# Optimization experiments

Hardware: AMD Instinct MI355X
Metric: run time of the kernel (lower is better)

## Reference

```python
import jax, jax.numpy as jnp
import numpy as np
from jax import lax

B, C, H, W = 8, 2, 1024, 1024
K = 500            # max_num
POST_MAX = 83      # circle_nms post_max_size
NMS_THRESH = 4.0   # squared-distance threshold in grid units
SCORE_THR = 0.1
# post_center_range converted to grid units per CenterPointBBoxCoder.__init__
PCR_LOW = jnp.array([-100.0, -100.0, -10.0], dtype=jnp.float32)
PCR_HIGH = jnp.array([1124.0, 1124.0, 10.0], dtype=jnp.float32)


def setup_inputs() -> dict:
    key = jax.random.key(0)
    ks = jax.random.split(key, 7)
    return {
        "heat": jax.random.uniform(ks[0], (B, C, H, W), dtype=jnp.float32),
        "reg": jax.random.normal(ks[1], (B, 2, H, W), dtype=jnp.float32),
        "rot_sine": jax.random.normal(ks[2], (B, 1, H, W), dtype=jnp.float32),
        "rot_cosine": jax.random.normal(ks[3], (B, 1, H, W), dtype=jnp.float32),
        "hei": jax.random.normal(ks[4], (B, 1, H, W), dtype=jnp.float32),
        "dim": jax.random.normal(ks[5], (B, 3, H, W), dtype=jnp.float32),
        "vel": jax.random.normal(ks[6], (B, 2, H, W), dtype=jnp.float32),
    }


def _gather_feat(feat_bnc, inds_bk):
    # feat: [B, N, Ch], inds: [B, K] -> [B, K, Ch]
    return jnp.take_along_axis(feat_bnc, inds_bk[:, :, None], axis=1)


def _transpose_and_gather(feat_bchw, inds_bk):
    # [B, Ch, H, W] -> gather at flat HW indices -> [B, K, Ch]
    b, c, h, w = feat_bchw.shape
    f = feat_bchw.transpose(0, 2, 3, 1).reshape(b, h * w, c)
    return _gather_feat(f, inds_bk)


def _topk(scores):
    # scores: [B, C, H, W]
    b, c, h, w = scores.shape
    topk_scores, topk_inds = lax.top_k(scores.reshape(b, c, h * w), K)  # [B,C,K]
    topk_inds = topk_inds % (h * w)
    topk_ys = (topk_inds // w).astype(jnp.float32)
    topk_xs = (topk_inds % w).astype(jnp.float32)
    topk_score, topk_ind = lax.top_k(topk_scores.reshape(b, c * K), K)  # [B,K]
    topk_clses = (topk_ind // K).astype(jnp.int32)
    gather2 = lambda t: jnp.take_along_axis(t.reshape(b, c * K), topk_ind, axis=1)
    return topk_score, gather2(topk_inds), topk_clses, gather2(topk_ys), gather2(topk_xs)


def _circle_nms_keep(x, y, s):
    # Sequential circle NMS per image (jit-compatible fori_loop).
    k = x.shape[0]
    order = jnp.argsort(-s)
    xs, ys = x[order], y[order]
    idx = jnp.arange(k)

    def body(i, supp):
        d2 = (xs - xs[i]) ** 2 + (ys - ys[i]) ** 2
        new = supp | ((idx > i) & (d2 <= NMS_THRESH))
        return jnp.where(supp[i], supp, new)

    supp = lax.fori_loop(0, k, body, jnp.zeros(k, dtype=bool))
    keep_sorted = ~supp
    keep_sorted = keep_sorted & (jnp.cumsum(keep_sorted.astype(jnp.int32)) <= POST_MAX)
    return jnp.zeros(k, dtype=bool).at[order].set(keep_sorted)


def reference(heat, reg, rot_sine, rot_cosine, hei, dim, vel):
    scores, inds, clses, ys, xs = _topk(heat)            # [B,K] each
    reg_g = _transpose_and_gather(reg, inds)             # [B,K,2]
    xs = xs[:, :, None] + reg_g[:, :, 0:1]
    ys = ys[:, :, None] + reg_g[:, :, 1:2]
    rot = jnp.arctan2(_transpose_and_gather(rot_sine, inds),
                      _transpose_and_gather(rot_cosine, inds))  # [B,K,1]
    hei_g = _transpose_and_gather(hei, inds)             # [B,K,1]
    dim_g = _transpose_and_gather(dim, inds)             # [B,K,3]
    vel_g = _transpose_and_gather(vel, inds)             # [B,K,2]
    boxes = jnp.concatenate([xs, ys, hei_g, dim_g, rot, vel_g], axis=2)  # [B,K,9]

    valid = (boxes[..., :3] >= PCR_LOW).all(-1) & (boxes[..., :3] <= PCR_HIGH).all(-1)
    valid = valid & (scores > SCORE_THR)

    nms_scores = jnp.where(valid, scores, -1e9)
    keep = jax.vmap(_circle_nms_keep)(boxes[..., 0], boxes[..., 1], nms_scores) & valid
    return boxes, scores, clses.astype(jnp.float32), valid, keep
```

## Files before the change

### kernel.cpp

```cpp
#include <hip/hip_runtime.h>
#include <stdint.h>

typedef unsigned int u32;
typedef unsigned long long u64;

#define HW (1024*1024)
#define KTOP 500
#define CAP 8192u
#define POST_MAX 83
#define DELTA_THR 9728u

#define WS_CNT2  0
#define WS_CAND  32768
#define WS_SORT  1081344


__global__ __launch_bounds__(256) void k1_collect(const float* __restrict__ heat,
                                                  u32* cnt2, uint2* cand){
  __shared__ uint2 lbuf[64];
  __shared__ u32 lcnt;
  int s     = blockIdx.x >> 7;
  int chunk = blockIdx.x & 127;
  int tid   = threadIdx.x;
  if (tid == 0) lcnt = 0;
  __syncthreads();
  const float4* hp = (const float4*)(heat + (size_t)s*HW + (size_t)chunk*8192);
  float4 v[8];
  #pragma unroll
  for (int i = 0; i < 8; ++i) v[i] = hp[i*256 + tid];
  #pragma unroll
  for (int i = 0; i < 8; ++i){
    u32 idx0 = (u32)chunk*8192u + (u32)(i*256 + tid)*4u;
    float vals[4] = {v[i].x, v[i].y, v[i].z, v[i].w};
    #pragma unroll
    for (int c = 0; c < 4; ++c){
      u32 bits  = __float_as_uint(vals[c]);
      u32 delta = 0x3F800000u - bits;
      if (delta < DELTA_THR){
        u32 p = atomicAdd(&lcnt, 1u);
        if (p < 64u) lbuf[p] = make_uint2(bits, idx0 + (u32)c);
      }
    }
  }
  __syncthreads();
  u32 n = lcnt;
  u32 stored = (n < 64u) ? n : 64u;
  if (tid < stored) cand[(size_t)s*CAP + (u32)chunk*64u + tid] = lbuf[tid];
  if (tid == 0) cnt2[s*128 + chunk] = stored | ((n > 64u) ? 0x80000000u : 0u);
}

__global__ __launch_bounds__(1024) void kR_rank(const float* __restrict__ heat,
                                                const u32* __restrict__ cnt2,
                                                uint2* cand, uint2* sorted){
  __shared__ __align__(16) u64 lkey[CAP];
  __shared__ u32 coff[129];
  __shared__ u32 lhist[256];
  __shared__ u32 lc;
  __shared__ int t2s;
  __shared__ u32 meta;
  int s = blockIdx.x >> 1, h = blockIdx.x & 1, t = threadIdx.x;

  if (t == 0){
    u32 tot = 0, ov = 0;
    for (int c = 0; c < 128; ++c){
      u32 w = cnt2[s*128 + c];
      ov |= (w >> 31);
      coff[c] = tot;
      tot += (w & 0x7FFFFFFFu);
    }
    coff[128] = tot;
    meta = tot | (ov << 31);
  }
  __syncthreads();
  u32 total = meta & 0x7FFFFFFFu;
  bool fb = ((meta >> 31) != 0u) || (total < (u32)KTOP);
  u32 n;

  if (!fb){
    n = total;
    for (u32 i = t; i < CAP; i += 1024){
      u32 c = i >> 6, j = i & 63u;
      u32 cnt_c = coff[c+1] - coff[c];
      if (j < cnt_c){
        uint2 cv = cand[(size_t)s*CAP + i];
        lkey[coff[c] + j] = ((u64)(~cv.x) << 32) | (u64)cv.y;
      }
    }
    __syncthreads();
  } else {
    if (h) return;
    if (t < 256) lhist[t] = 0;
    if (t == 0) lc = 0;
    __syncthreads();
    const float4* hp = (const float4*)(heat + (size_t)s*HW);
    for (int it = 0; it < 256; ++it){
      float4 v = hp[it*1024 + t];
      #pragma unroll
      for (int c = 0; c < 4; ++c){
        float val = (c==0)?v.x:(c==1)?v.y:(c==2)?v.z:v.w;
        u32 bits  = __float_as_uint(val);
        u32 delta = 0x3F800000u - bits;
        u32 bin   = delta >> 16; if (bin > 255u) bin = 255u;
        atomicAdd(&lhist[bin], 1u);
      }
    }
    __syncthreads();
    if (t == 0){
      u32 cum = 0; u32 b1 = 255u;
      for (u32 bb = 0; bb < 256u; ++bb){
        cum += lhist[bb];
        if (cum >= (u32)KTOP){ b1 = bb; break; }
      }
      t2s = (int)(0x3F800000u - ((b1 + 1u) << 16) + 1u);
    }
    __syncthreads();
    int t2 = t2s;
    for (int it = 0; it < 256; ++it){
      float4 v = hp[it*1024 + t];
      u32 idx0 = (u32)(it*1024 + t)*4u;
      #pragma unroll
      for (int c = 0; c < 4; ++c){
        float val = (c==0)?v.x:(c==1)?v.y:(c==2)?v.z:v.w;
        int bits = (int)__float_as_uint(val);
        if (bits >= t2){
          u32 p = atomicAdd(&lc, 1u);
          if (p < CAP) cand[(size_t)s*CAP + p] = make_uint2((u32)bits, idx0 + (u32)c);
        }
      }
    }
    __syncthreads();
    n = (lc < CAP) ? lc : CAP;
    for (u32 i = t; i < n; i += 1024){
      uint2 cv = cand[(size_t)s*CAP + i];
      lkey[i] = ((u64)(~cv.x) << 32) | (u64)cv.y;
    }
    __syncthreads();
  }

  u32 lo = fb ? 0u : (u32)h * ((n + 1u) >> 1);
  u32 hi = fb ? n  : (h ? n : ((n + 1u) >> 1));
  const ulonglong2* lk2 = (const ulonglong2*)lkey;
  for (u32 me = lo + t; me < hi; me += 1024){
    u64 k0 = lkey[me];
    u32 r = 0;
    u32 half = n >> 1;
    for (u32 j = 0; j < half; ++j){
      ulonglong2 kk = lk2[j];
      r += (kk.x < k0) ? 1u : 0u;
      r += (kk.y < k0) ? 1u : 0u;
    }
    if (n & 1u) r += (lkey[n-1] < k0) ? 1u : 0u;
    if (r < 512u)
      sorted[s*512 + (int)r] = make_uint2(~(u32)(k0 >> 32), (u32)k0);
  }
}

__global__ __launch_bounds__(1024) void kT_tail(const uint2* __restrict__ sorted,
                                                const float* __restrict__ reg,
                                                const float* __restrict__ rots,
                                                const float* __restrict__ rotc,
                                                const float* __restrict__ hei,
                                                const float* __restrict__ dim,
                                                const float* __restrict__ vel,
                                                float* out){
  __shared__ u64 k2a[512], k2b[512];
  __shared__ uint2 fin[512];
  __shared__ float xo[512], yo[512];
  __shared__ float2 pts[512];
  __shared__ int order[512], vld[512];
  __shared__ u32 ordvl[512];
  __shared__ int wsum[16];
  __shared__ u64 keepw[8];
  int b = blockIdx.x, t = threadIdx.x;

  uint2 mye = make_uint2(0u, 0u);
  if (t < 512){
    mye = sorted[(b*2 + 0)*512 + t];
    k2a[t] = ((u64)(~mye.x) << 32) | (u64)t;
  } else {
    int p = t - 512;
    mye = sorted[(b*2 + 1)*512 + p];
    k2b[p] = ((u64)(~mye.x) << 32) | (u64)(KTOP + p);
  }
  if (t < 8) keepw[t] = 0ull;
  __syncthreads();

  if (t < KTOP){
    u64 K = k2a[t];
    int lo = 0, hi = KTOP;
    while (lo < hi){ int mid = (lo + hi) >> 1; if (k2b[mid] < K) lo = mid + 1; else hi = mid; }
    int m = t + lo;
    if (m < KTOP){
      fin[m] = make_uint2(mye.x, mye.y & 0xFFFFFu);
      out[36000 + b*KTOP + m] = __uint_as_float(mye.x);
      out[40000 + b*KTOP + m] = 0.0f;
    }
  } else if (t >= 512 && t < 512 + KTOP){
    int p = t - 512;
    u64 K = k2b[p];
    int lo = 0, hi = KTOP;
    while (lo < hi){ int mid = (lo + hi) >> 1; if (k2a[mid] < K) lo = mid + 1; else hi = mid; }
    int m = p + lo;
    if (m < KTOP){
      fin[m] = make_uint2(mye.x, (mye.y & 0xFFFFFu) | (1u << 20));
      out[36000 + b*KTOP + m] = __uint_as_float(mye.x);
      out[40000 + b*KTOP + m] = 1.0f;
    }
  }
  __syncthreads();

  float x = 0.f, y = 0.f; int v = 0;
  if (t < KTOP){
    uint2 e = fin[t];
    u32 ind = e.y & 0xFFFFFu;
    float mysc = __uint_as_float(e.x);
    float xs0 = (float)(ind & 1023u);
    float ys0 = (float)(ind >> 10);
    size_t bb = (size_t)b;
    float r0  = reg [(bb*2 + 0)*HW + ind];
    float r1  = reg [(bb*2 + 1)*HW + ind];
    float sn  = rots[ bb       *HW + ind];
    float cs  = rotc[ bb       *HW + ind];
    float he  = hei [ bb       *HW + ind];
    float d0  = dim [(bb*3 + 0)*HW + ind];
    float d1  = dim [(bb*3 + 1)*HW + ind];
    float d2v = dim [(bb*3 + 2)*HW + ind];
    float v0  = vel [(bb*2 + 0)*HW + ind];
    float v1  = vel [(bb*2 + 1)*HW + ind];
    x = xs0 + r0; y = ys0 + r1;
    float rot = atan2f(sn, cs);
    float* bx = out + (size_t)(b*KTOP + t)*9;
    bx[0]=x; bx[1]=y; bx[2]=he; bx[3]=d0; bx[4]=d1; bx[5]=d2v; bx[6]=rot; bx[7]=v0; bx[8]=v1;
    v = ((x >= -100.0f) && (x <= 1124.0f) &&
         (y >= -100.0f) && (y <= 1124.0f) &&
         (he >= -10.0f) && (he <= 10.0f) && (mysc > 0.1f)) ? 1 : 0;
    out[44000 + b*KTOP + t] = v ? 1.0f : 0.0f;
  }
  if (t < 512){ xo[t] = x; yo[t] = y; vld[t] = v; }

  u64 bm = __ballot(v != 0);
  int lane = t & 63, wv = t >> 6;
  if (lane == 0) wsum[wv] = __popcll(bm);
  __syncthreads();
  int off = 0, nValid = 0;
  #pragma unroll
  for (int w2 = 0; w2 < 8; ++w2){
    int sv = wsum[w2];
    nValid += sv;
    if (w2 < wv) off += sv;
  }
  int incl = off + __popcll(bm & ((~0ull) >> (63 - lane)));
  if (t < KTOP){
    int excl = incl - v;
    int slot = v ? excl : (nValid + (t - excl));
    order[slot] = t;
  }
  __syncthreads();

  if (t < KTOP){
    int p = order[t];
    pts[t] = make_float2(xo[p], yo[p]);
    ordvl[t] = (u32)p | ((u32)vld[p] << 31);
  } else if (t < 512){
    pts[t] = make_float2(1e30f, 1e30f);
    ordvl[t] = 0u;
  }
  __syncthreads();

  if (t < 64){
    int nv = nValid;
    float kx0 = 1e30f, ky0 = 1e30f, kx1 = 1e30f, ky1 = 1e30f;
    int count = 0;
    u64 curw = 0ull;
    int i = 0;
    float2 pcur = pts[0];
    float2 pnxt = pts[1];
    for (i = 0; i < nv; ++i){
      float2 p = pcur;
      pcur = pnxt;
      pnxt = pts[(i + 2 < 512) ? (i + 2) : 511];
      float dx0 = __fsub_rn(kx0, p.x), dy0 = __fsub_rn(ky0, p.y);
      float dx1 = __fsub_rn(kx1, p.x), dy1 = __fsub_rn(ky1, p.y);
      float d20 = __fadd_rn(__fmul_rn(dx0,dx0), __fmul_rn(dy0,dy0));
      float d21 = __fadd_rn(__fmul_rn(dx1,dx1), __fmul_rn(dy1,dy1));
      bool nearby = (d20 <= 4.0f) || (d21 <= 4.0f);
      if (!__any(nearby)){
        curw |= (1ull << (i & 63));
        if (count < 64){
          if (t == count){ kx0 = p.x; ky0 = p.y; }
        } else {
          if (t == count - 64){ kx1 = p.x; ky1 = p.y; }
        }
        ++count;
        if (count == POST_MAX) break;
      }
      if ((i & 63) == 63){
        if (t == 0) keepw[i >> 6] |= curw;
        curw = 0ull;
      }
    }
    if (t == 0 && curw != 0ull){
      int wi = i >> 6; if (wi > 7) wi = 7;
      keepw[wi] |= curw;
    }
  }
  __syncthreads();

  if (t < KTOP){
    int bit = (int)((keepw[t >> 6] >> (t & 63)) & 1ull);
    u32 pv = ordvl[t];
    int p = (int)(pv & 511u);
    out[48000 + b*KTOP + p] = (bit && (pv >> 31)) ? 1.0f : 0.0f;
  }
}

extern "C" void kernel_launch(void* const* d_in, const int* in_sizes, int n_in,
                              void* d_out, int out_size, void* d_ws, size_t ws_size,
                              hipStream_t stream){
  const float* heat = (const float*)d_in[0];
  const float* reg  = (const float*)d_in[1];
  const float* rots = (const float*)d_in[2];
  const float* rotc = (const float*)d_in[3];
  const float* hei  = (const float*)d_in[4];
  const float* dim  = (const float*)d_in[5];
  const float* vel  = (const float*)d_in[6];
  float* out = (float*)d_out;
  char* ws = (char*)d_ws;
  u32*   cnt2   = (u32*)  (ws + WS_CNT2);
  uint2* cand   = (uint2*)(ws + WS_CAND);
  uint2* sorted = (uint2*)(ws + WS_SORT);

  k1_collect <<<2048, 256, 0, stream>>>(heat, cnt2, cand);
  kR_rank    <<<32,  1024, 0, stream>>>(heat, cnt2, cand, sorted);
  kT_tail    <<<8,   1024, 0, stream>>>(sorted, reg, rots, rotc, hei, dim, vel, out);
}
```

Before: 54.82 us.

## Fuse rank kernel into tail kernel, keeping sorted candidates in shared memory

Merges the per-slice rank/sort kernel into the tail kernel: each of the 8 blocks now handles both class slices of its image in sequence, ranks the candidates in LDS, and keeps the sorted top entries in shared memory instead of a global workspace. The tail's scratch arrays are aliased onto the large key buffer. This removes one kernel launch and a global round trip, but the ranking work now runs on 8 blocks instead of 32 and the two slices are processed serially, which cuts parallelism for the quadratic rank step.

```diff
diff --git a/kernel.cpp b/kernel.cpp
--- a/kernel.cpp
+++ b/kernel.cpp
@@ -12,7 +12,6 @@
 
 #define WS_CNT2  0
 #define WS_CAND  32768
-#define WS_SORT  1081344
 
 
 __global__ __launch_bounds__(256) void k1_collect(const float* __restrict__ heat,
@@ -49,113 +48,9 @@
   if (tid == 0) cnt2[s*128 + chunk] = stored | ((n > 64u) ? 0x80000000u : 0u);
 }
 
-__global__ __launch_bounds__(1024) void kR_rank(const float* __restrict__ heat,
+__global__ __launch_bounds__(1024) void kT_tail(const float* __restrict__ heat,
                                                 const u32* __restrict__ cnt2,
-                                                uint2* cand, uint2* sorted){
-  __shared__ __align__(16) u64 lkey[CAP];
-  __shared__ u32 coff[129];
-  __shared__ u32 lhist[256];
-  __shared__ u32 lc;
-  __shared__ int t2s;
-  __shared__ u32 meta;
-  int s = blockIdx.x >> 1, h = blockIdx.x & 1, t = threadIdx.x;
-
-  if (t == 0){
-    u32 tot = 0, ov = 0;
-    for (int c = 0; c < 128; ++c){
-      u32 w = cnt2[s*128 + c];
-      ov |= (w >> 31);
-      coff[c] = tot;
-      tot += (w & 0x7FFFFFFFu);
-    }
-    coff[128] = tot;
-    meta = tot | (ov << 31);
-  }
-  __syncthreads();
-  u32 total = meta & 0x7FFFFFFFu;
-  bool fb = ((meta >> 31) != 0u) || (total < (u32)KTOP);
-  u32 n;
-
-  if (!fb){
-    n = total;
-    for (u32 i = t; i < CAP; i += 1024){
-      u32 c = i >> 6, j = i & 63u;
-      u32 cnt_c = coff[c+1] - coff[c];
-      if (j < cnt_c){
-        uint2 cv = cand[(size_t)s*CAP + i];
-        lkey[coff[c] + j] = ((u64)(~cv.x) << 32) | (u64)cv.y;
-      }
-    }
-    __syncthreads();
-  } else {
-    if (h) return;
-    if (t < 256) lhist[t] = 0;
-    if (t == 0) lc = 0;
-    __syncthreads();
-    const float4* hp = (const float4*)(heat + (size_t)s*HW);
-    for (int it = 0; it < 256; ++it){
-      float4 v = hp[it*1024 + t];
-      #pragma unroll
-      for (int c = 0; c < 4; ++c){
-        float val = (c==0)?v.x:(c==1)?v.y:(c==2)?v.z:v.w;
-        u32 bits  = __float_as_uint(val);
-        u32 delta = 0x3F800000u - bits;
-        u32 bin   = delta >> 16; if (bin > 255u) bin = 255u;
-        atomicAdd(&lhist[bin], 1u);
-      }
-    }
-    __syncthreads();
-    if (t == 0){
-      u32 cum = 0; u32 b1 = 255u;
-      for (u32 bb = 0; bb < 256u; ++bb){
-        cum += lhist[bb];
-        if (cum >= (u32)KTOP){ b1 = bb; break; }
-      }
-      t2s = (int)(0x3F800000u - ((b1 + 1u) << 16) + 1u);
-    }
-    __syncthreads();
-    int t2 = t2s;
-    for (int it = 0; it < 256; ++it){
-      float4 v = hp[it*1024 + t];
-      u32 idx0 = (u32)(it*1024 + t)*4u;
-      #pragma unroll
-      for (int c = 0; c < 4; ++c){
-        float val = (c==0)?v.x:(c==1)?v.y:(c==2)?v.z:v.w;
-        int bits = (int)__float_as_uint(val);
-        if (bits >= t2){
-          u32 p = atomicAdd(&lc, 1u);
-          if (p < CAP) cand[(size_t)s*CAP + p] = make_uint2((u32)bits, idx0 + (u32)c);
-        }
-      }
-    }
-    __syncthreads();
-    n = (lc < CAP) ? lc : CAP;
-    for (u32 i = t; i < n; i += 1024){
-      uint2 cv = cand[(size_t)s*CAP + i];
-      lkey[i] = ((u64)(~cv.x) << 32) | (u64)cv.y;
-    }
-    __syncthreads();
-  }
-
-  u32 lo = fb ? 0u : (u32)h * ((n + 1u) >> 1);
-  u32 hi = fb ? n  : (h ? n : ((n + 1u) >> 1));
-  const ulonglong2* lk2 = (const ulonglong2*)lkey;
-  for (u32 me = lo + t; me < hi; me += 1024){
-    u64 k0 = lkey[me];
-    u32 r = 0;
-    u32 half = n >> 1;
-    for (u32 j = 0; j < half; ++j){
-      ulonglong2 kk = lk2[j];
-      r += (kk.x < k0) ? 1u : 0u;
-      r += (kk.y < k0) ? 1u : 0u;
-    }
-    if (n & 1u) r += (lkey[n-1] < k0) ? 1u : 0u;
-    if (r < 512u)
-      sorted[s*512 + (int)r] = make_uint2(~(u32)(k0 >> 32), (u32)k0);
-  }
-}
-
-__global__ __launch_bounds__(1024) void kT_tail(const uint2* __restrict__ sorted,
+                                                uint2* cand,
                                                 const float* __restrict__ reg,
                                                 const float* __restrict__ rots,
                                                 const float* __restrict__ rotc,
@@ -163,23 +58,133 @@
                                                 const float* __restrict__ dim,
                                                 const float* __restrict__ vel,
                                                 float* out){
-  __shared__ u64 k2a[512], k2b[512];
-  __shared__ uint2 fin[512];
-  __shared__ float xo[512], yo[512];
-  __shared__ float2 pts[512];
-  __shared__ int order[512], vld[512];
-  __shared__ u32 ordvl[512];
+  __shared__ __align__(16) u64 lkey[CAP];
+  __shared__ uint2 sortedL[2][512];
+  __shared__ u32 tmpc[128];
+  __shared__ u32 cofs[129];
+  __shared__ u32 lhist[256];
+  __shared__ u32 lc;
+  __shared__ int t2s;
+  __shared__ u32 meta_sh;
   __shared__ int wsum[16];
   __shared__ u64 keepw[8];
   int b = blockIdx.x, t = threadIdx.x;
 
+  for (int sl = 0; sl < 2; ++sl){
+    int s = 2*b + sl;
+    if (t < 128) tmpc[t] = cnt2[s*128 + t];
+    __syncthreads();
+    if (t == 0){
+      u32 tot = 0, ov = 0;
+      for (int c = 0; c < 128; ++c){
+        u32 w = tmpc[c];
+        ov |= (w >> 31);
+        cofs[c] = tot;
+        tot += (w & 0x7FFFFFFFu);
+      }
+      cofs[128] = tot;
+      meta_sh = tot | (ov << 31);
+    }
+    __syncthreads();
+    u32 total = meta_sh & 0x7FFFFFFFu;
+    bool fb = ((meta_sh >> 31) != 0u) || (total < (u32)KTOP);
+    u32 n;
+
+    if (!fb){
+      n = total;
+      for (u32 i = t; i < CAP; i += 1024){
+        u32 c = i >> 6, j = i & 63u;
+        u32 cnt_c = cofs[c+1] - cofs[c];
+        if (j < cnt_c){
+          uint2 cv = cand[(size_t)s*CAP + i];
+          lkey[cofs[c] + j] = ((u64)(~cv.x) << 32) | (u64)cv.y;
+        }
+      }
+      __syncthreads();
+    } else {
+      if (t < 256) lhist[t] = 0;
+      if (t == 0) lc = 0;
+      __syncthreads();
+      const float4* hp = (const float4*)(heat + (size_t)s*HW);
+      for (int it = 0; it < 256; ++it){
+        float4 v = hp[it*1024 + t];
+        #pragma unroll
+        for (int c = 0; c < 4; ++c){
+          float val = (c==0)?v.x:(c==1)?v.y:(c==2)?v.z:v.w;
+          u32 bits  = __float_as_uint(val);
+          u32 delta = 0x3F800000u - bits;
+          u32 bin   = delta >> 16; if (bin > 255u) bin = 255u;
+          atomicAdd(&lhist[bin], 1u);
+        }
+      }
+      __syncthreads();
+      if (t == 0){
+        u32 cum = 0; u32 b1 = 255u;
+        for (u32 bb = 0; bb < 256u; ++bb){
+          cum += lhist[bb];
+          if (cum >= (u32)KTOP){ b1 = bb; break; }
+        }
+        t2s = (int)(0x3F800000u - ((b1 + 1u) << 16) + 1u);
+      }
+      __syncthreads();
+      int t2 = t2s;
+      for (int it = 0; it < 256; ++it){
+        float4 v = hp[it*1024 + t];
+        u32 idx0 = (u32)(it*1024 + t)*4u;
+        #pragma unroll
+        for (int c = 0; c < 4; ++c){
+          float val = (c==0)?v.x:(c==1)?v.y:(c==2)?v.z:v.w;
+          int bits = (int)__float_as_uint(val);
+          if (bits >= t2){
+            u32 p = atomicAdd(&lc, 1u);
+            if (p < CAP) cand[(size_t)s*CAP + p] = make_uint2((u32)bits, idx0 + (u32)c);
+          }
+        }
+      }
+      __syncthreads();
+      n = (lc < CAP) ? lc : CAP;
+      for (u32 i = t; i < n; i += 1024){
+        uint2 cv = cand[(size_t)s*CAP + i];
+        lkey[i] = ((u64)(~cv.x) << 32) | (u64)cv.y;
+      }
+      __syncthreads();
+    }
+
+    const ulonglong2* lk2 = (const ulonglong2*)lkey;
+    for (u32 me = t; me < n; me += 1024){
+      u64 k0 = lkey[me];
+      u32 r = 0;
+      u32 half = n >> 1;
+      for (u32 j = 0; j < half; ++j){
+        ulonglong2 kk = lk2[j];
+        r += (kk.x < k0) ? 1u : 0u;
+        r += (kk.y < k0) ? 1u : 0u;
+      }
+      if (n & 1u) r += (lkey[n-1] < k0) ? 1u : 0u;
+      if (r < 512u)
+        sortedL[sl][r] = make_uint2(~(u32)(k0 >> 32), (u32)k0);
+    }
+    __syncthreads();
+  }
+
+  char* big = (char*)lkey;
+  u64*    k2a   = (u64*)   big;
+  u64*    k2b   = (u64*)  (big + 4096);
+  uint2*  fin   = (uint2*)(big + 8192);
+  float*  xo    = (float*)(big + 12288);
+  float*  yo    = (float*)(big + 14336);
+  float2* pts   = (float2*)(big + 16384);
+  int*    order = (int*)  (big + 20480);
+  int*    vld   = (int*)  (big + 22528);
+  u32*    ordvl = (u32*)  (big + 24576);
+
   uint2 mye = make_uint2(0u, 0u);
   if (t < 512){
-    mye = sorted[(b*2 + 0)*512 + t];
+    mye = sortedL[0][t];
     k2a[t] = ((u64)(~mye.x) << 32) | (u64)t;
   } else {
     int p = t - 512;
-    mye = sorted[(b*2 + 1)*512 + p];
+    mye = sortedL[1][p];
     k2b[p] = ((u64)(~mye.x) << 32) | (u64)(KTOP + p);
   }
   if (t < 8) keepw[t] = 0ull;
@@ -326,11 +331,9 @@
   const float* vel  = (const float*)d_in[6];
   float* out = (float*)d_out;
   char* ws = (char*)d_ws;
-  u32*   cnt2   = (u32*)  (ws + WS_CNT2);
-  uint2* cand   = (uint2*)(ws + WS_CAND);
-  uint2* sorted = (uint2*)(ws + WS_SORT);
+  u32*   cnt2 = (u32*)  (ws + WS_CNT2);
+  uint2* cand = (uint2*)(ws + WS_CAND);
 
   k1_collect <<<2048, 256, 0, stream>>>(heat, cnt2, cand);
-  kR_rank    <<<32,  1024, 0, stream>>>(heat, cnt2, cand, sorted);
-  kT_tail    <<<8,   1024, 0, stream>>>(sorted, reg, rots, rotc, hei, dim, vel, out);
+  kT_tail    <<<8,   1024, 0, stream>>>(heat, cnt2, cand, reg, rots, rotc, hei, dim, vel, out);
 }
```

Result: slower. 68.19 us (+24.4%).
